# Kernel tuning notes

Hardware: AMD Instinct MI355X
Metric: run time of the kernel (lower is better)

Reference implementation:

```python
import jax, jax.numpy as jnp
import numpy as np

VOCAB, HID, EMB, KSZ, VSZ = 34, 512, 128, 128, 128
T, N, L = 1024, 128, 200


def setup_inputs() -> dict:
    key = jax.random.key(0)
    ks = jax.random.split(key, 20)
    s = 0.05
    emb = jax.random.normal(ks[0], (VOCAB, EMB), jnp.float32) * s
    emb = emb.at[0].set(0.0)  # padding_idx=0
    inp = {
        "key_proj": jax.random.normal(ks[1], (T, N, KSZ), jnp.float32),
        "values": jax.random.normal(ks[2], (T, N, VSZ), jnp.float32),
        "reduced_length": jax.random.randint(ks[3], (N,), 1, T + 1),
        "text": jax.random.randint(ks[4], (N, L), 1, VOCAB),
        "embedding": emb,
        "Wq": jax.random.normal(ks[5], (KSZ, EMB), jnp.float32) * s,
        "bq": jnp.zeros((KSZ,), jnp.float32),
        "W_ih1": jax.random.normal(ks[6], (4 * HID, EMB + VSZ), jnp.float32) * s,
        "W_hh1": jax.random.normal(ks[7], (4 * HID, HID), jnp.float32) * s,
        "b_ih1": jnp.zeros((4 * HID,), jnp.float32),
        "b_hh1": jnp.zeros((4 * HID,), jnp.float32),
        "W_ih2": jax.random.normal(ks[8], (4 * KSZ, HID), jnp.float32) * s,
        "W_hh2": jax.random.normal(ks[9], (4 * KSZ, KSZ), jnp.float32) * s,
        "b_ih2": jnp.zeros((4 * KSZ,), jnp.float32),
        "b_hh2": jnp.zeros((4 * KSZ,), jnp.float32),
        "Wfc": jax.random.normal(ks[10], (EMB, KSZ * 2), jnp.float32) * s,
        "bfc": jnp.zeros((EMB,), jnp.float32),
        "b_out": jnp.zeros((VOCAB,), jnp.float32),
    }
    return inp


def _lstm_cell(x, h, c, Wih, Whh, bih, bhh):
    g = x @ Wih.T + bih + h @ Whh.T + bhh
    i, f, gg, o = jnp.split(g, 4, axis=1)
    c = jax.nn.sigmoid(f) * c + jax.nn.sigmoid(i) * jnp.tanh(gg)
    h = jax.nn.sigmoid(o) * jnp.tanh(c)
    return h, c


def reference(key_proj, values, reduced_length, text, embedding, Wq, bq,
              W_ih1, W_hh1, b_ih1, b_hh1, W_ih2, W_hh2, b_ih2, b_hh2,
              Wfc, bfc, b_out):
    n, l = text.shape
    keyT = jnp.transpose(key_proj, (1, 0, 2))   # (N,T,K)
    valT = jnp.transpose(values, (1, 0, 2))     # (N,T,V)
    t_len = keyT.shape[1]
    mask = jnp.arange(t_len)[None, :] >= reduced_length[:, None]  # (N,T) True=pad

    def attend(q):  # q: (N,K)
        energy = jnp.einsum('ntk,nk->nt', keyT, q)
        energy = jnp.where(mask, -1e9, energy)
        att = jax.nn.softmax(energy, axis=1)
        ctx = jnp.einsum('nt,ntv->nv', att, valT)
        return ctx

    # deterministic teacher forcing: step 0 uses embedding[0] (padding row),
    # step i uses embedding of text[:, i-1]
    char_seq = jnp.concatenate(
        [jnp.broadcast_to(embedding[0], (n, 1, embedding.shape[1])),
         embedding[text[:, :-1]]], axis=1)          # (N,L,E)
    char_seq = jnp.transpose(char_seq, (1, 0, 2))   # (L,N,E)

    h1 = jnp.zeros((n, W_hh1.shape[1]), jnp.float32)
    c1 = jnp.zeros_like(h1)
    h2 = jnp.zeros((n, W_hh2.shape[1]), jnp.float32)
    c2 = jnp.zeros_like(h2)

    def step(carry, ce):
        h1, c1, h2, c2 = carry
        q1 = ce @ Wq.T + bq
        ctx1 = attend(q1)
        inp = jnp.concatenate([ce, ctx1], axis=1)
        h1, c1 = _lstm_cell(inp, h1, c1, W_ih1, W_hh1, b_ih1, b_hh1)
        h2, c2 = _lstm_cell(h1, h2, c2, W_ih2, W_hh2, b_ih2, b_hh2)
        q2 = h2 @ Wq.T + bq
        ctx2 = attend(q2)
        out = jnp.concatenate([h2, ctx2], axis=1) @ Wfc.T + bfc
        out = jnp.clip(out, -1.0, 1.0)  # Hardtanh
        pred = out @ embedding.T + b_out  # tied output weights
        return (h1, c1, h2, c2), pred

    _, preds = jax.lax.scan(step, (h1, c1, h2, c2), char_seq)  # (L,N,V)
    return jnp.transpose(preds, (1, 0, 2))  # (N,L,V)
```

## Files before the change

### kernel.cpp

```cpp
#include <hip/hip_runtime.h>
#include <hip/hip_bf16.h>
#include <math.h>

#define T_LEN 1024
#define NB    128
#define L_SEQ 200
#define EMB   128
#define KSZ   128
#define VSZ   128
#define HID   512
#define G1    2048
#define G2    512
#define VOCAB 34
#define KK1   768
#define KK2   640
#define TT    64
#define NBLK  160
#define GRP_BLKS 40

typedef __attribute__((ext_vector_type(8))) short bf16x8;
typedef __attribute__((ext_vector_type(4))) float f32x4;

__device__ __forceinline__ float sig_(float x) { return 1.0f / (1.0f + __expf(-x)); }
__device__ __forceinline__ float tanh_fast(float x) {
    return 1.0f - 2.0f / (__expf(2.0f * x) + 1.0f);
}

__device__ __forceinline__ f32x4 MFMA_BF16(bf16x8 a, bf16x8 b, f32x4 c) {
    return __builtin_amdgcn_mfma_f32_16x16x32_bf16(a, b, c, 0, 0, 0);
}
__device__ __forceinline__ bf16x8 LD8(const __hip_bfloat16* p) {
    return *(const bf16x8*)p;
}
__device__ __forceinline__ bf16x8 LD8CC(const unsigned int* p) {
    union { bf16x8 v; unsigned long long q[2]; } u;
    unsigned long long* pp = (unsigned long long*)p;
    u.q[0] = __hip_atomic_load(pp,     __ATOMIC_RELAXED, __HIP_MEMORY_SCOPE_AGENT);
    u.q[1] = __hip_atomic_load(pp + 1, __ATOMIC_RELAXED, __HIP_MEMORY_SCOPE_AGENT);
    return u.v;
}
__device__ __forceinline__ void ST4CC(unsigned int* p, unsigned int v) {
    __hip_atomic_store(p, v, __ATOMIC_RELAXED, __HIP_MEMORY_SCOPE_AGENT);
}

__device__ __forceinline__ void gbar_grp(int* bar, int tgt) {
    asm volatile("s_waitcnt vmcnt(0)" ::: "memory");
    __syncthreads();
    if (threadIdx.x == 0) {
        __hip_atomic_fetch_add(bar, 1, __ATOMIC_RELAXED, __HIP_MEMORY_SCOPE_AGENT);
        const long long t0 = __builtin_amdgcn_s_memrealtime();
        while (__hip_atomic_load(bar, __ATOMIC_RELAXED, __HIP_MEMORY_SCOPE_AGENT) < tgt) {
            __builtin_amdgcn_s_sleep(2);
            if (__builtin_amdgcn_s_memrealtime() - t0 > 2000000LL) break;
        }
    }
    __syncthreads();
}

__global__ __launch_bounds__(256) void prep_kernel(
    const float* __restrict__ Wih1, const float* __restrict__ Whh1,
    const float* __restrict__ bih1, const float* __restrict__ bhh1,
    const float* __restrict__ Wih2, const float* __restrict__ Whh2,
    const float* __restrict__ bih2, const float* __restrict__ bhh2,
    __hip_bfloat16* __restrict__ Wc1, __hip_bfloat16* __restrict__ Wc2,
    float* __restrict__ bb1, float* __restrict__ bb2,
    unsigned int* __restrict__ h1x, unsigned int* __restrict__ h2x,
    int* __restrict__ bar)
{
    const int gid = blockIdx.x * 256 + threadIdx.x;
    if (gid < G1 * KK1) {
        const int o = gid / KK1, k = gid - o * KK1;
        const float v = (k < 256) ? Wih1[o * 256 + k] : Whh1[o * 512 + (k - 256)];
        Wc1[gid] = __float2bfloat16(v);
    }
    if (gid < G2 * KK2) {
        const int o = gid / KK2, k = gid - o * KK2;
        const float v = (k < 512) ? Wih2[o * 512 + k] : Whh2[o * 128 + (k - 512)];
        Wc2[gid] = __float2bfloat16(v);
    }
    if (gid < G1) bb1[gid] = bih1[gid] + bhh1[gid];
    if (gid < G2) bb2[gid] = bih2[gid] + bhh2[gid];
    if (gid < 2 * NB * HID / 2) h1x[gid] = 0u;
    if (gid < 2 * NB * KSZ / 2) h2x[gid] = 0u;
    if (gid < 256) bar[gid] = 0;
}

__global__ __launch_bounds__(256) void ce_gather(
    const int* __restrict__ text, const float* __restrict__ emb,
    float* __restrict__ ce_f, __hip_bfloat16* __restrict__ ce_b)
{
    const int idx = blockIdx.x * 256 + threadIdx.x;
    const int k = idx & 127;
    const int rn = idx >> 7;
    const int nn = rn & 127;
    const int s = rn >> 7;
    if (s >= L_SEQ) return;
    const int tok = (s == 0) ? 0 : text[nn * L_SEQ + (s - 1)];
    const float v = emb[(size_t)tok * EMB + k];
    ce_f[idx] = v;
    ce_b[idx] = __float2bfloat16(v);
}

__global__ __launch_bounds__(256) void qproj_kernel(
    const float* __restrict__ src, const float* __restrict__ Wq,
    const float* __restrict__ bq, float* __restrict__ dst)
{
    __shared__ float xs[2][KSZ];
    const int tid = threadIdx.x;
    const int r0 = blockIdx.x * 2;
    xs[tid >> 7][tid & 127] = src[(size_t)(r0 + (tid >> 7)) * KSZ + (tid & 127)];
    __syncthreads();
    const int sub = tid >> 7, o = tid & 127;
    const float* wr = Wq + (size_t)o * KSZ;
    float acc = bq[o];
    #pragma unroll 8
    for (int k = 0; k < KSZ; k += 4) {
        const float4 w4 = *(const float4*)&wr[k];
        const float4 x4 = *(const float4*)&xs[sub][k];
        acc += w4.x * x4.x + w4.y * x4.y + w4.z * x4.z + w4.w * x4.w;
    }
    dst[(size_t)(r0 + sub) * KSZ + o] = acc;
}

__global__ __launch_bounds__(256) void attn_kernel(
    const float* __restrict__ q,
    const float* __restrict__ key,
    const float* __restrict__ values,
    const int* __restrict__ rlen,
    float* __restrict__ ctx_f,
    __hip_bfloat16* __restrict__ ctx_b)
{
    __shared__ __align__(16) float q_s[52][128];
    __shared__ __align__(16) float Kt[TT][129];
    __shared__ __align__(16) float Vt[TT][129];
    __shared__ __align__(16) float es[52][68];
    __shared__ float mm[52], ss[52], al[52];
    const int tid = threadIdx.x;
    const int n = blockIdx.x >> 2;
    const int l0 = (blockIdx.x & 3) * 50;
    const int len = rlen[n];

    for (int idx = tid; idx < 52 * 128; idx += 256) {
        const int l = idx >> 7, k = idx & 127;
        q_s[l][k] = (l < 50) ? q[((size_t)(l0 + l) * NB + n) * KSZ + k] : 0.0f;
    }
    for (int l = tid; l < 52; l += 256) { mm[l] = -3.0e38f; ss[l] = 0.0f; }
    float acc[25];
    #pragma unroll
    for (int j = 0; j < 25; ++j) acc[j] = 0.0f;
    __syncthreads();

    const int lg = tid >> 6, lane = tid & 63;
    const int vv = tid & 127, hh = tid >> 7;
    const int nt = (len + TT - 1) / TT;

    for (int tt = 0; tt < nt; ++tt) {
        const int tb = tt * TT;
        const int valid = min(TT, len - tb);
        #pragma unroll
        for (int it = 0; it < 8; ++it) {
            const int idx4 = tid + it * 256;
            const int r = idx4 >> 5, c4 = (idx4 & 31) * 4;
            float4 kq = make_float4(0.f, 0.f, 0.f, 0.f);
            float4 vq = make_float4(0.f, 0.f, 0.f, 0.f);
            if (r < valid) {
                const size_t base = ((size_t)(tb + r) * NB + n) * 128 + c4;
                kq = *(const float4*)&key[base];
                vq = *(const float4*)&values[base];
            }
            Kt[r][c4 + 0] = kq.x; Kt[r][c4 + 1] = kq.y;
            Kt[r][c4 + 2] = kq.z; Kt[r][c4 + 3] = kq.w;
            Vt[r][c4 + 0] = vq.x; Vt[r][c4 + 1] = vq.y;
            Vt[r][c4 + 2] = vq.z; Vt[r][c4 + 3] = vq.w;
        }
        __syncthreads();
        {
            float e[13];
            #pragma unroll
            for (int j = 0; j < 13; ++j) e[j] = 0.0f;
            for (int k4 = 0; k4 < 128; k4 += 4) {
                const float c0 = Kt[lane][k4 + 0], c1 = Kt[lane][k4 + 1];
                const float c2 = Kt[lane][k4 + 2], c3 = Kt[lane][k4 + 3];
                #pragma unroll
                for (int j = 0; j < 13; ++j) {
                    const float4 q4 = *(const float4*)&q_s[lg * 13 + j][k4];
                    e[j] += c0 * q4.x + c1 * q4.y + c2 * q4.z + c3 * q4.w;
                }
            }
            #pragma unroll
            for (int j = 0; j < 13; ++j) {
                const int l = lg * 13 + j;
                float ev = (lane < valid) ? e[j] : -3.0e38f;
                #pragma unroll
                for (int off = 32; off; off >>= 1) ev = fmaxf(ev, __shfl_xor(ev, off, 64));
                const float mold = mm[l];
                const float mnew = fmaxf(mold, ev);
                const float p = (lane < valid) ? __expf(e[j] - mnew) : 0.0f;
                es[l][lane] = p;
                float ps = p;
                #pragma unroll
                for (int off = 32; off; off >>= 1) ps += __shfl_xor(ps, off, 64);
                if (lane == 0) {
                    const float a = __expf(mold - mnew);
                    al[l] = a;
                    ss[l] = ss[l] * a + ps;
                    mm[l] = mnew;
                }
            }
        }
        __syncthreads();
        #pragma unroll
        for (int j = 0; j < 25; ++j) {
            const int l = hh + 2 * j;
            float a = acc[j] * al[l];
            #pragma unroll 4
            for (int t4 = 0; t4 < TT; t4 += 4) {
                const float4 p4 = *(const float4*)&es[l][t4];
                a += p4.x * Vt[t4 + 0][vv] + p4.y * Vt[t4 + 1][vv]
                   + p4.z * Vt[t4 + 2][vv] + p4.w * Vt[t4 + 3][vv];
            }
            acc[j] = a;
        }
        __syncthreads();
    }
    #pragma unroll
    for (int j = 0; j < 25; ++j) {
        const int l = hh + 2 * j;
        const float r = acc[j] / ss[l];
        const size_t o = ((size_t)(l0 + l) * NB + n) * VSZ + vv;
        ctx_f[o] = r;
        ctx_b[o] = __float2bfloat16(r);
    }
}

__global__ __launch_bounds__(256) void scan_persist(
    const __hip_bfloat16* __restrict__ Wc1, const __hip_bfloat16* __restrict__ Wc2,
    const float* __restrict__ bb1, const float* __restrict__ bb2,
    const __hip_bfloat16* __restrict__ ce_b, const __hip_bfloat16* __restrict__ ctx1_b,
    unsigned int* __restrict__ h1x, unsigned int* __restrict__ h2x,
    float* __restrict__ h2_all, int* __restrict__ bar)
{
    const int tid = threadIdx.x;
    const int w = tid >> 6;
    const int lane = tid & 63;
    const int lrow = lane & 15;
    const int krow = (lane >> 4) * 8;
    __shared__ float gl[4][32][65];
    const int nl = tid >> 3, op = tid & 7;

    if (blockIdx.x < 32) {
        const int grp = blockIdx.x >> 3;
        int* gb = bar + grp * 64;
        const int n0 = grp * 32;
        const int og = blockIdx.x & 7;
        const int wbase = w * 160;
        bf16x8 wf[20];
        #pragma unroll
        for (int t = 0; t < 4; ++t)
            #pragma unroll
            for (int j = 0; j < 5; ++j)
                wf[t * 5 + j] = LD8(Wc2 + (size_t)(t * 128 + og * 16 + lrow) * KK2
                                        + wbase + j * 32 + krow);
        const int oc = og * 16 + 2 * op;
        float bia[4][2];
        #pragma unroll
        for (int g = 0; g < 4; ++g) {
            bia[g][0] = bb2[g * 128 + oc];
            bia[g][1] = bb2[g * 128 + oc + 1];
        }
        float cst0 = 0.0f, cst1 = 0.0f;
        for (int i = 0; i <= L_SEQ; ++i) {
            if (i >= 1) {
                const int s2 = i - 1;
                const int rb = i & 1;
                const unsigned int* h1r = h1x + rb * (NB * HID / 2);
                const unsigned int* h2r = h2x + rb * (NB * KSZ / 2);
                unsigned int* h2w = h2x + (rb ^ 1) * (NB * KSZ / 2);
                f32x4 acc0[4] = {{0,0,0,0},{0,0,0,0},{0,0,0,0},{0,0,0,0}};
                f32x4 acc1[4] = {{0,0,0,0},{0,0,0,0},{0,0,0,0},{0,0,0,0}};
                #pragma unroll
                for (int j = 0; j < 5; ++j) {
                    const int kg = wbase + j * 32 + krow;
                    bf16x8 a0, a1;
                    if (kg < 512) {
                        a0 = LD8CC(h1r + (n0 + lrow) * (HID / 2) + kg / 2);
                        a1 = LD8CC(h1r + (n0 + lrow + 16) * (HID / 2) + kg / 2);
                    } else {
                        a0 = LD8CC(h2r + (n0 + lrow) * (KSZ / 2) + (kg - 512) / 2);
                        a1 = LD8CC(h2r + (n0 + lrow + 16) * (KSZ / 2) + (kg - 512) / 2);
                    }
                    #pragma unroll
                    for (int t = 0; t < 4; ++t) {
                        acc0[t] = MFMA_BF16(a0, wf[t * 5 + j], acc0[t]);
                        acc1[t] = MFMA_BF16(a1, wf[t * 5 + j], acc1[t]);
                    }
                }
                const int rbase = (lane >> 4) * 4;
                #pragma unroll
                for (int t = 0; t < 4; ++t)
                    #pragma unroll
                    for (int r = 0; r < 4; ++r) {
                        gl[w][rbase + r][t * 16 + lrow] = acc0[t][r];
                        gl[w][16 + rbase + r][t * 16 + lrow] = acc1[t][r];
                    }
                __syncthreads();
                float hv0, hv1;
                {
                    float sg[4][2];
                    #pragma unroll
                    for (int g = 0; g < 4; ++g)
                        #pragma unroll
                        for (int cc = 0; cc < 2; ++cc)
                            sg[g][cc] = gl[0][nl][g * 16 + 2 * op + cc]
                                      + gl[1][nl][g * 16 + 2 * op + cc]
                                      + gl[2][nl][g * 16 + 2 * op + cc]
                                      + gl[3][nl][g * 16 + 2 * op + cc] + bia[g][cc];
                    const float cn0 = sig_(sg[1][0]) * cst0 + sig_(sg[0][0]) * tanh_fast(sg[2][0]);
                    const float cn1 = sig_(sg[1][1]) * cst1 + sig_(sg[0][1]) * tanh_fast(sg[2][1]);
                    hv0 = sig_(sg[3][0]) * tanh_fast(cn0);
                    hv1 = sig_(sg[3][1]) * tanh_fast(cn1);
                    cst0 = cn0; cst1 = cn1;
                }
                const int nn = n0 + nl;
                union { unsigned int u; __hip_bfloat16 b[2]; } pk;
                pk.b[0] = __float2bfloat16(hv0);
                pk.b[1] = __float2bfloat16(hv1);
                ST4CC(h2w + nn * (KSZ / 2) + oc / 2, pk.u);
                *(float2*)&h2_all[((size_t)s2 * NB + nn) * KSZ + oc] = make_float2(hv0, hv1);
            }
            if (i < L_SEQ) gbar_grp(gb, GRP_BLKS * (i + 1));
        }
    } else {
        const int bid2 = blockIdx.x - 32;
        const int grp = bid2 >> 5;
        int* gb = bar + grp * 64;
        const int n0 = grp * 32;
        const int og = bid2 & 31;
        const int wbase = w * 192;
        bf16x8 wf[24];
        #pragma unroll
        for (int t = 0; t < 4; ++t)
            #pragma unroll
            for (int j = 0; j < 6; ++j)
                wf[t * 6 + j] = LD8(Wc1 + (size_t)(t * 512 + og * 16 + lrow) * KK1
                                        + wbase + j * 32 + krow);
        const int oc = og * 16 + 2 * op;
        float bia[4][2];
        #pragma unroll
        for (int g = 0; g < 4; ++g) {
            bia[g][0] = bb1[g * 512 + oc];
            bia[g][1] = bb1[g * 512 + oc + 1];
        }
        float cst0 = 0.0f, cst1 = 0.0f;
        for (int i = 0; i < L_SEQ; ++i) {
            const int rb = i & 1;
            const unsigned int* h1r = h1x + rb * (NB * HID / 2);
            unsigned int* h1w = h1x + (rb ^ 1) * (NB * HID / 2);
            f32x4 acc0[4] = {{0,0,0,0},{0,0,0,0},{0,0,0,0},{0,0,0,0}};
            f32x4 acc1[4] = {{0,0,0,0},{0,0,0,0},{0,0,0,0},{0,0,0,0}};
            #pragma unroll
            for (int j = 0; j < 6; ++j) {
                const int kg = wbase + j * 32 + krow;
                bf16x8 a0, a1;
                if (kg < 128) {
                    a0 = LD8(ce_b + ((size_t)i * NB + n0 + lrow) * EMB + kg);
                    a1 = LD8(ce_b + ((size_t)i * NB + n0 + lrow + 16) * EMB + kg);
                } else if (kg < 256) {
                    a0 = LD8(ctx1_b + ((size_t)i * NB + n0 + lrow) * VSZ + kg - 128);
                    a1 = LD8(ctx1_b + ((size_t)i * NB + n0 + lrow + 16) * VSZ + kg - 128);
                } else {
                    a0 = LD8CC(h1r + (n0 + lrow) * (HID / 2) + (kg - 256) / 2);
                    a1 = LD8CC(h1r + (n0 + lrow + 16) * (HID / 2) + (kg - 256) / 2);
                }
                #pragma unroll
                for (int t = 0; t < 4; ++t) {
                    acc0[t] = MFMA_BF16(a0, wf[t * 6 + j], acc0[t]);
                    acc1[t] = MFMA_BF16(a1, wf[t * 6 + j], acc1[t]);
                }
            }
            const int rbase = (lane >> 4) * 4;
            #pragma unroll
            for (int t = 0; t < 4; ++t)
                #pragma unroll
                for (int r = 0; r < 4; ++r) {
                    gl[w][rbase + r][t * 16 + lrow] = acc0[t][r];
                    gl[w][16 + rbase + r][t * 16 + lrow] = acc1[t][r];
                }
            __syncthreads();
            float hv0, hv1;
            {
                float sg[4][2];
                #pragma unroll
                for (int g = 0; g < 4; ++g)
                    #pragma unroll
                    for (int cc = 0; cc < 2; ++cc)
                        sg[g][cc] = gl[0][nl][g * 16 + 2 * op + cc]
                                  + gl[1][nl][g * 16 + 2 * op + cc]
                                  + gl[2][nl][g * 16 + 2 * op + cc]
                                  + gl[3][nl][g * 16 + 2 * op + cc] + bia[g][cc];
                const float cn0 = sig_(sg[1][0]) * cst0 + sig_(sg[0][0]) * tanh_fast(sg[2][0]);
                const float cn1 = sig_(sg[1][1]) * cst1 + sig_(sg[0][1]) * tanh_fast(sg[2][1]);
                hv0 = sig_(sg[3][0]) * tanh_fast(cn0);
                hv1 = sig_(sg[3][1]) * tanh_fast(cn1);
                cst0 = cn0; cst1 = cn1;
            }
            union { unsigned int u; __hip_bfloat16 b[2]; } pk;
            pk.b[0] = __float2bfloat16(hv0);
            pk.b[1] = __float2bfloat16(hv1);
            ST4CC(h1w + (n0 + nl) * (HID / 2) + oc / 2, pk.u);
            gbar_grp(gb, GRP_BLKS * (i + 1));
        }
    }
}

__global__ __launch_bounds__(256) void outpred_kernel(
    const float* __restrict__ h2_all, const float* __restrict__ ctx2,
    const float* __restrict__ Wfc, const float* __restrict__ bfc,
    const float* __restrict__ emb, const float* __restrict__ b_out,
    float* __restrict__ out)
{
    __shared__ float xs[2][256];
    __shared__ float os[2][EMB];
    const int tid = threadIdx.x;
    const int r0 = blockIdx.x * 2;
    const int sub = tid >> 7, lane = tid & 127;
    const int r = r0 + sub;
    xs[sub][lane] = h2_all[(size_t)r * KSZ + lane];
    xs[sub][128 + lane] = ctx2[(size_t)r * VSZ + lane];
    __syncthreads();
    const float* wr = Wfc + (size_t)lane * 256;
    float acc = bfc[lane];
    #pragma unroll 8
    for (int k = 0; k < 256; k += 4) {
        const float4 w4 = *(const float4*)&wr[k];
        const float4 x4 = *(const float4*)&xs[sub][k];
        acc += w4.x * x4.x + w4.y * x4.y + w4.z * x4.z + w4.w * x4.w;
    }
    acc = fminf(1.0f, fmaxf(-1.0f, acc));
    os[sub][lane] = acc;
    __syncthreads();
    if (lane < VOCAB) {
        const float* er = emb + (size_t)lane * EMB;
        float a = b_out[lane];
        #pragma unroll 8
        for (int e = 0; e < EMB; e += 4) {
            const float4 e4 = *(const float4*)&er[e];
            const float4 x4 = *(const float4*)&os[sub][e];
            a += e4.x * x4.x + e4.y * x4.y + e4.z * x4.z + e4.w * x4.w;
        }
        const int s = r >> 7, nn = r & 127;
        out[((size_t)nn * L_SEQ + s) * VOCAB + lane] = a;
    }
}

extern "C" void kernel_launch(void* const* d_in, const int* in_sizes, int n_in,
                              void* d_out, int out_size, void* d_ws, size_t ws_size,
                              hipStream_t stream)
{
    (void)in_sizes; (void)n_in; (void)out_size; (void)ws_size;
    const float* key_proj = (const float*)d_in[0];
    const float* values   = (const float*)d_in[1];
    const int*   rlen     = (const int*)d_in[2];
    const int*   text     = (const int*)d_in[3];
    const float* emb      = (const float*)d_in[4];
    const float* Wq    = (const float*)d_in[5];
    const float* bq    = (const float*)d_in[6];
    const float* Wih1  = (const float*)d_in[7];
    const float* Whh1  = (const float*)d_in[8];
    const float* bih1  = (const float*)d_in[9];
    const float* bhh1  = (const float*)d_in[10];
    const float* Wih2  = (const float*)d_in[11];
    const float* Whh2  = (const float*)d_in[12];
    const float* bih2  = (const float*)d_in[13];
    const float* bhh2  = (const float*)d_in[14];
    const float* Wfc   = (const float*)d_in[15];
    const float* bfc   = (const float*)d_in[16];
    const float* b_out = (const float*)d_in[17];
    float* out = (float*)d_out;

    char* p = (char*)d_ws;
    auto take = [&p](size_t bytes) -> char* {
        char* r = p;
        p += (bytes + 255) & ~((size_t)255);
        return r;
    };
    float* ce_f  = (float*)take((size_t)L_SEQ * NB * EMB * 4);
    __hip_bfloat16* ce_b  = (__hip_bfloat16*)take((size_t)L_SEQ * NB * EMB * 2);
    __hip_bfloat16* ctx_b = (__hip_bfloat16*)take((size_t)L_SEQ * NB * VSZ * 2);
    float* ctx_f  = (float*)take((size_t)L_SEQ * NB * VSZ * 4);
    float* qbuf   = (float*)take((size_t)L_SEQ * NB * KSZ * 4);
    float* h2_all = (float*)take((size_t)L_SEQ * NB * KSZ * 4);
    __hip_bfloat16* Wc1 = (__hip_bfloat16*)take((size_t)G1 * KK1 * 2);
    __hip_bfloat16* Wc2 = (__hip_bfloat16*)take((size_t)G2 * KK2 * 2);
    float* bb1 = (float*)take(G1 * 4);
    float* bb2 = (float*)take(G2 * 4);
    unsigned int* h1x = (unsigned int*)take((size_t)2 * NB * HID / 2 * 4);
    unsigned int* h2x = (unsigned int*)take((size_t)2 * NB * KSZ / 2 * 4);
    int* bar = (int*)take(1024);

    prep_kernel<<<6144, 256, 0, stream>>>(Wih1, Whh1, bih1, bhh1, Wih2, Whh2,
                                          bih2, bhh2, Wc1, Wc2, bb1, bb2,
                                          h1x, h2x, bar);
    ce_gather<<<12800, 256, 0, stream>>>(text, emb, ce_f, ce_b);
    qproj_kernel<<<12800, 256, 0, stream>>>(ce_f, Wq, bq, qbuf);
    attn_kernel<<<512, 256, 0, stream>>>(qbuf, key_proj, values, rlen, ctx_f, ctx_b);
    scan_persist<<<NBLK, 256, 0, stream>>>(Wc1, Wc2, bb1, bb2, ce_b, ctx_b,
                                           h1x, h2x, h2_all, bar);
    qproj_kernel<<<12800, 256, 0, stream>>>(h2_all, Wq, bq, qbuf);
    attn_kernel<<<512, 256, 0, stream>>>(qbuf, key_proj, values, rlen, ctx_f, ctx_b);
    outpred_kernel<<<12800, 256, 0, stream>>>(h2_all, ctx_f, Wfc, bfc, emb, b_out, out);
}
```

Measured before the change: 3.770 ms.

## Replace group barrier with split producer/consumer counters in persistent LSTM scan

The single 40-block group barrier in the persistent scan is replaced by per-subgroup arrival counters. Layer-1 blocks signal one of four counters, layer-2 blocks signal read-done and write-done counters, and each side spins only on the counters it depends on. Layer-1 blocks now prefetch the non-recurrent ce/ctx operands before waiting, and the K-split across warps is reorganised so each warp loads its recurrent slice up front. The attention PV loop is also reordered so each V value is loaded once and reused across 25 rows. This loosens the lockstep between layers to hide synchronisation latency, at the cost of more complex counter protocols and more atomic polling.

```diff
diff --git a/kernel.cpp b/kernel.cpp
--- a/kernel.cpp
+++ b/kernel.cpp
@@ -16,7 +16,6 @@
 #define KK2   640
 #define TT    64
 #define NBLK  160
-#define GRP_BLKS 40
 
 typedef __attribute__((ext_vector_type(8))) short bf16x8;
 typedef __attribute__((ext_vector_type(4))) float f32x4;
@@ -25,7 +24,6 @@
 __device__ __forceinline__ float tanh_fast(float x) {
     return 1.0f - 2.0f / (__expf(2.0f * x) + 1.0f);
 }
-
 __device__ __forceinline__ f32x4 MFMA_BF16(bf16x8 a, bf16x8 b, f32x4 c) {
     return __builtin_amdgcn_mfma_f32_16x16x32_bf16(a, b, c, 0, 0, 0);
 }
@@ -42,19 +40,21 @@
 __device__ __forceinline__ void ST4CC(unsigned int* p, unsigned int v) {
     __hip_atomic_store(p, v, __ATOMIC_RELAXED, __HIP_MEMORY_SCOPE_AGENT);
 }
-
-__device__ __forceinline__ void gbar_grp(int* bar, int tgt) {
-    asm volatile("s_waitcnt vmcnt(0)" ::: "memory");
-    __syncthreads();
-    if (threadIdx.x == 0) {
-        __hip_atomic_fetch_add(bar, 1, __ATOMIC_RELAXED, __HIP_MEMORY_SCOPE_AGENT);
-        const long long t0 = __builtin_amdgcn_s_memrealtime();
-        while (__hip_atomic_load(bar, __ATOMIC_RELAXED, __HIP_MEMORY_SCOPE_AGENT) < tgt) {
-            __builtin_amdgcn_s_sleep(2);
-            if (__builtin_amdgcn_s_memrealtime() - t0 > 2000000LL) break;
-        }
-    }
-    __syncthreads();
+__device__ __forceinline__ void CADD(int* p) {
+    __hip_atomic_fetch_add(p, 1, __ATOMIC_RELAXED, __HIP_MEMORY_SCOPE_AGENT);
+}
+__device__ __forceinline__ void spinw(int* gb, int t1, int tR, int slotR) {
+    const long long t0 = __builtin_amdgcn_s_memrealtime();
+    for (;;) {
+        const int a = __hip_atomic_load(gb +   0, __ATOMIC_RELAXED, __HIP_MEMORY_SCOPE_AGENT);
+        const int b = __hip_atomic_load(gb +  64, __ATOMIC_RELAXED, __HIP_MEMORY_SCOPE_AGENT);
+        const int c = __hip_atomic_load(gb + 128, __ATOMIC_RELAXED, __HIP_MEMORY_SCOPE_AGENT);
+        const int d = __hip_atomic_load(gb + 192, __ATOMIC_RELAXED, __HIP_MEMORY_SCOPE_AGENT);
+        const int r = __hip_atomic_load(gb + slotR * 64, __ATOMIC_RELAXED, __HIP_MEMORY_SCOPE_AGENT);
+        if (a >= t1 && b >= t1 && c >= t1 && d >= t1 && r >= tR) return;
+        __builtin_amdgcn_s_sleep(1);
+        if (__builtin_amdgcn_s_memrealtime() - t0 > 2000000LL) return;
+    }
 }
 
 __global__ __launch_bounds__(256) void prep_kernel(
@@ -82,7 +82,7 @@
     if (gid < G2) bb2[gid] = bih2[gid] + bhh2[gid];
     if (gid < 2 * NB * HID / 2) h1x[gid] = 0u;
     if (gid < 2 * NB * KSZ / 2) h2x[gid] = 0u;
-    if (gid < 256) bar[gid] = 0;
+    if (gid < 2048) bar[gid] = 0;
 }
 
 __global__ __launch_bounds__(256) void ce_gather(
@@ -210,16 +210,15 @@
         }
         __syncthreads();
         #pragma unroll
-        for (int j = 0; j < 25; ++j) {
-            const int l = hh + 2 * j;
-            float a = acc[j] * al[l];
-            #pragma unroll 4
-            for (int t4 = 0; t4 < TT; t4 += 4) {
-                const float4 p4 = *(const float4*)&es[l][t4];
-                a += p4.x * Vt[t4 + 0][vv] + p4.y * Vt[t4 + 1][vv]
-                   + p4.z * Vt[t4 + 2][vv] + p4.w * Vt[t4 + 3][vv];
-            }
-            acc[j] = a;
+        for (int j = 0; j < 25; ++j) acc[j] *= al[hh + 2 * j];
+        for (int t4 = 0; t4 < TT; t4 += 4) {
+            const float v0 = Vt[t4 + 0][vv], v1 = Vt[t4 + 1][vv];
+            const float v2 = Vt[t4 + 2][vv], v3 = Vt[t4 + 3][vv];
+            #pragma unroll
+            for (int j = 0; j < 25; ++j) {
+                const float4 p4 = *(const float4*)&es[hh + 2 * j][t4];
+                acc[j] += p4.x * v0 + p4.y * v1 + p4.z * v2 + p4.w * v3;
+            }
         }
         __syncthreads();
     }
@@ -245,22 +244,23 @@
     const int lane = tid & 63;
     const int lrow = lane & 15;
     const int krow = (lane >> 4) * 8;
-    __shared__ float gl[4][32][65];
+    const int rbase = (lane >> 4) * 4;
+    __shared__ float gl[4][32][68];
     const int nl = tid >> 3, op = tid & 7;
 
     if (blockIdx.x < 32) {
         const int grp = blockIdx.x >> 3;
-        int* gb = bar + grp * 64;
+        int* gb = bar + grp * 6 * 64;
         const int n0 = grp * 32;
         const int og = blockIdx.x & 7;
-        const int wbase = w * 160;
         bf16x8 wf[20];
         #pragma unroll
         for (int t = 0; t < 4; ++t)
             #pragma unroll
-            for (int j = 0; j < 5; ++j)
-                wf[t * 5 + j] = LD8(Wc2 + (size_t)(t * 128 + og * 16 + lrow) * KK2
-                                        + wbase + j * 32 + krow);
+            for (int j = 0; j < 5; ++j) {
+                const int kk = (j < 4) ? (w * 128 + j * 32 + krow) : (512 + w * 32 + krow);
+                wf[t * 5 + j] = LD8(Wc2 + (size_t)(t * 128 + og * 16 + lrow) * KK2 + kk);
+            }
         const int oc = og * 16 + 2 * op;
         float bia[4][2];
         #pragma unroll
@@ -269,116 +269,41 @@
             bia[g][1] = bb2[g * 128 + oc + 1];
         }
         float cst0 = 0.0f, cst1 = 0.0f;
-        for (int i = 0; i <= L_SEQ; ++i) {
-            if (i >= 1) {
-                const int s2 = i - 1;
-                const int rb = i & 1;
-                const unsigned int* h1r = h1x + rb * (NB * HID / 2);
-                const unsigned int* h2r = h2x + rb * (NB * KSZ / 2);
-                unsigned int* h2w = h2x + (rb ^ 1) * (NB * KSZ / 2);
-                f32x4 acc0[4] = {{0,0,0,0},{0,0,0,0},{0,0,0,0},{0,0,0,0}};
-                f32x4 acc1[4] = {{0,0,0,0},{0,0,0,0},{0,0,0,0},{0,0,0,0}};
-                #pragma unroll
-                for (int j = 0; j < 5; ++j) {
-                    const int kg = wbase + j * 32 + krow;
-                    bf16x8 a0, a1;
-                    if (kg < 512) {
-                        a0 = LD8CC(h1r + (n0 + lrow) * (HID / 2) + kg / 2);
-                        a1 = LD8CC(h1r + (n0 + lrow + 16) * (HID / 2) + kg / 2);
-                    } else {
-                        a0 = LD8CC(h2r + (n0 + lrow) * (KSZ / 2) + (kg - 512) / 2);
-                        a1 = LD8CC(h2r + (n0 + lrow + 16) * (KSZ / 2) + (kg - 512) / 2);
-                    }
-                    #pragma unroll
-                    for (int t = 0; t < 4; ++t) {
-                        acc0[t] = MFMA_BF16(a0, wf[t * 5 + j], acc0[t]);
-                        acc1[t] = MFMA_BF16(a1, wf[t * 5 + j], acc1[t]);
-                    }
-                }
-                const int rbase = (lane >> 4) * 4;
-                #pragma unroll
-                for (int t = 0; t < 4; ++t)
-                    #pragma unroll
-                    for (int r = 0; r < 4; ++r) {
-                        gl[w][rbase + r][t * 16 + lrow] = acc0[t][r];
-                        gl[w][16 + rbase + r][t * 16 + lrow] = acc1[t][r];
-                    }
-                __syncthreads();
-                float hv0, hv1;
-                {
-                    float sg[4][2];
-                    #pragma unroll
-                    for (int g = 0; g < 4; ++g)
-                        #pragma unroll
-                        for (int cc = 0; cc < 2; ++cc)
-                            sg[g][cc] = gl[0][nl][g * 16 + 2 * op + cc]
-                                      + gl[1][nl][g * 16 + 2 * op + cc]
-                                      + gl[2][nl][g * 16 + 2 * op + cc]
-                                      + gl[3][nl][g * 16 + 2 * op + cc] + bia[g][cc];
-                    const float cn0 = sig_(sg[1][0]) * cst0 + sig_(sg[0][0]) * tanh_fast(sg[2][0]);
-                    const float cn1 = sig_(sg[1][1]) * cst1 + sig_(sg[0][1]) * tanh_fast(sg[2][1]);
-                    hv0 = sig_(sg[3][0]) * tanh_fast(cn0);
-                    hv1 = sig_(sg[3][1]) * tanh_fast(cn1);
-                    cst0 = cn0; cst1 = cn1;
-                }
-                const int nn = n0 + nl;
-                union { unsigned int u; __hip_bfloat16 b[2]; } pk;
-                pk.b[0] = __float2bfloat16(hv0);
-                pk.b[1] = __float2bfloat16(hv1);
-                ST4CC(h2w + nn * (KSZ / 2) + oc / 2, pk.u);
-                *(float2*)&h2_all[((size_t)s2 * NB + nn) * KSZ + oc] = make_float2(hv0, hv1);
-            }
-            if (i < L_SEQ) gbar_grp(gb, GRP_BLKS * (i + 1));
-        }
-    } else {
-        const int bid2 = blockIdx.x - 32;
-        const int grp = bid2 >> 5;
-        int* gb = bar + grp * 64;
-        const int n0 = grp * 32;
-        const int og = bid2 & 31;
-        const int wbase = w * 192;
-        bf16x8 wf[24];
-        #pragma unroll
-        for (int t = 0; t < 4; ++t)
-            #pragma unroll
-            for (int j = 0; j < 6; ++j)
-                wf[t * 6 + j] = LD8(Wc1 + (size_t)(t * 512 + og * 16 + lrow) * KK1
-                                        + wbase + j * 32 + krow);
-        const int oc = og * 16 + 2 * op;
-        float bia[4][2];
-        #pragma unroll
-        for (int g = 0; g < 4; ++g) {
-            bia[g][0] = bb1[g * 512 + oc];
-            bia[g][1] = bb1[g * 512 + oc + 1];
-        }
-        float cst0 = 0.0f, cst1 = 0.0f;
-        for (int i = 0; i < L_SEQ; ++i) {
-            const int rb = i & 1;
-            const unsigned int* h1r = h1x + rb * (NB * HID / 2);
-            unsigned int* h1w = h1x + (rb ^ 1) * (NB * HID / 2);
+        const unsigned int* h1e = h1x;
+        const unsigned int* h1o = h1x + NB * HID / 2;
+        const unsigned int* h2e = h2x;
+        const unsigned int* h2o = h2x + NB * KSZ / 2;
+        for (int i = 1; i <= L_SEQ; ++i) {
+            if (tid == 0) spinw(gb, 8 * i, 8 * (i - 1), 5);
+            __syncthreads();
+            const int s2 = i - 1;
+            const unsigned int* h1r = (i & 1) ? h1o : h1e;
+            const unsigned int* h2r = (i & 1) ? h2o : h2e;
+            unsigned int* h2w = (unsigned int*)((i & 1) ? h2e : h2o);
+            const unsigned int* r0 = h1r + (n0 + lrow) * (HID / 2) + (w * 128 + krow) / 2;
+            const unsigned int* r1 = h1r + (n0 + lrow + 16) * (HID / 2) + (w * 128 + krow) / 2;
+            const bf16x8 a00 = LD8CC(r0), a01 = LD8CC(r0 + 16), a02 = LD8CC(r0 + 32), a03 = LD8CC(r0 + 48);
+            const bf16x8 a10 = LD8CC(r1), a11 = LD8CC(r1 + 16), a12 = LD8CC(r1 + 32), a13 = LD8CC(r1 + 48);
+            const bf16x8 g0 = LD8CC(h2r + (n0 + lrow) * (KSZ / 2) + (w * 32 + krow) / 2);
+            const bf16x8 g1 = LD8CC(h2r + (n0 + lrow + 16) * (KSZ / 2) + (w * 32 + krow) / 2);
+            asm volatile("s_waitcnt vmcnt(0)" ::: "memory");
+            __syncthreads();
+            if (tid == 0) CADD(gb + 4 * 64);
             f32x4 acc0[4] = {{0,0,0,0},{0,0,0,0},{0,0,0,0},{0,0,0,0}};
             f32x4 acc1[4] = {{0,0,0,0},{0,0,0,0},{0,0,0,0},{0,0,0,0}};
             #pragma unroll
-            for (int j = 0; j < 6; ++j) {
-                const int kg = wbase + j * 32 + krow;
-                bf16x8 a0, a1;
-                if (kg < 128) {
-                    a0 = LD8(ce_b + ((size_t)i * NB + n0 + lrow) * EMB + kg);
-                    a1 = LD8(ce_b + ((size_t)i * NB + n0 + lrow + 16) * EMB + kg);
-                } else if (kg < 256) {
-                    a0 = LD8(ctx1_b + ((size_t)i * NB + n0 + lrow) * VSZ + kg - 128);
-                    a1 = LD8(ctx1_b + ((size_t)i * NB + n0 + lrow + 16) * VSZ + kg - 128);
-                } else {
-                    a0 = LD8CC(h1r + (n0 + lrow) * (HID / 2) + (kg - 256) / 2);
-                    a1 = LD8CC(h1r + (n0 + lrow + 16) * (HID / 2) + (kg - 256) / 2);
-                }
-                #pragma unroll
-                for (int t = 0; t < 4; ++t) {
-                    acc0[t] = MFMA_BF16(a0, wf[t * 6 + j], acc0[t]);
-                    acc1[t] = MFMA_BF16(a1, wf[t * 6 + j], acc1[t]);
-                }
-            }
-            const int rbase = (lane >> 4) * 4;
+            for (int t = 0; t < 4; ++t) {
+                acc0[t] = MFMA_BF16(a00, wf[t * 5 + 0], acc0[t]);
+                acc0[t] = MFMA_BF16(a01, wf[t * 5 + 1], acc0[t]);
+                acc0[t] = MFMA_BF16(a02, wf[t * 5 + 2], acc0[t]);
+                acc0[t] = MFMA_BF16(a03, wf[t * 5 + 3], acc0[t]);
+                acc0[t] = MFMA_BF16(g0,  wf[t * 5 + 4], acc0[t]);
+                acc1[t] = MFMA_BF16(a10, wf[t * 5 + 0], acc1[t]);
+                acc1[t] = MFMA_BF16(a11, wf[t * 5 + 1], acc1[t]);
+                acc1[t] = MFMA_BF16(a12, wf[t * 5 + 2], acc1[t]);
+                acc1[t] = MFMA_BF16(a13, wf[t * 5 + 3], acc1[t]);
+                acc1[t] = MFMA_BF16(g1,  wf[t * 5 + 4], acc1[t]);
+            }
             #pragma unroll
             for (int t = 0; t < 4; ++t)
                 #pragma unroll
@@ -387,28 +312,127 @@
                     gl[w][16 + rbase + r][t * 16 + lrow] = acc1[t][r];
                 }
             __syncthreads();
-            float hv0, hv1;
-            {
-                float sg[4][2];
+            float sg[4][2];
+            #pragma unroll
+            for (int g = 0; g < 4; ++g) {
+                float2 s0 = *(float2*)&gl[0][nl][g * 16 + 2 * op];
+                float2 s1 = *(float2*)&gl[1][nl][g * 16 + 2 * op];
+                float2 s2_ = *(float2*)&gl[2][nl][g * 16 + 2 * op];
+                float2 s3 = *(float2*)&gl[3][nl][g * 16 + 2 * op];
+                sg[g][0] = s0.x + s1.x + s2_.x + s3.x + bia[g][0];
+                sg[g][1] = s0.y + s1.y + s2_.y + s3.y + bia[g][1];
+            }
+            const float cn0 = sig_(sg[1][0]) * cst0 + sig_(sg[0][0]) * tanh_fast(sg[2][0]);
+            const float cn1 = sig_(sg[1][1]) * cst1 + sig_(sg[0][1]) * tanh_fast(sg[2][1]);
+            const float hv0 = sig_(sg[3][0]) * tanh_fast(cn0);
+            const float hv1 = sig_(sg[3][1]) * tanh_fast(cn1);
+            cst0 = cn0; cst1 = cn1;
+            const int nn = n0 + nl;
+            union { unsigned int u; __hip_bfloat16 b[2]; } pk;
+            pk.b[0] = __float2bfloat16(hv0);
+            pk.b[1] = __float2bfloat16(hv1);
+            ST4CC(h2w + nn * (KSZ / 2) + oc / 2, pk.u);
+            *(float2*)&h2_all[((size_t)s2 * NB + nn) * KSZ + oc] = make_float2(hv0, hv1);
+            asm volatile("s_waitcnt vmcnt(0)" ::: "memory");
+            __syncthreads();
+            if (tid == 0) CADD(gb + 5 * 64);
+        }
+    } else {
+        const int bid2 = blockIdx.x - 32;
+        const int grp = bid2 >> 5;
+        int* gb = bar + grp * 6 * 64;
+        const int n0 = grp * 32;
+        const int og = bid2 & 31;
+        int* myctr = gb + (og >> 3) * 64;
+        bf16x8 wf[24];
+        #pragma unroll
+        for (int t = 0; t < 4; ++t)
+            #pragma unroll
+            for (int j = 0; j < 6; ++j) {
+                const int kk = (j < 2) ? (w * 64 + j * 32 + krow)
+                                       : (256 + w * 128 + (j - 2) * 32 + krow);
+                wf[t * 6 + j] = LD8(Wc1 + (size_t)(t * 512 + og * 16 + lrow) * KK1 + kk);
+            }
+        const int oc = og * 16 + 2 * op;
+        float bia[4][2];
+        #pragma unroll
+        for (int g = 0; g < 4; ++g) {
+            bia[g][0] = bb1[g * 512 + oc];
+            bia[g][1] = bb1[g * 512 + oc + 1];
+        }
+        float cst0 = 0.0f, cst1 = 0.0f;
+        const unsigned int* h1e = h1x;
+        const unsigned int* h1o = h1x + NB * HID / 2;
+        for (int i = 0; i < L_SEQ; ++i) {
+            bf16x8 pj0h0, pj1h0, pj0h1, pj1h1;
+            if (w < 2) {
+                const __hip_bfloat16* s0 = ce_b + ((size_t)i * NB + n0 + lrow) * EMB + w * 64 + krow;
+                const __hip_bfloat16* s1 = ce_b + ((size_t)i * NB + n0 + lrow + 16) * EMB + w * 64 + krow;
+                pj0h0 = LD8(s0); pj1h0 = LD8(s0 + 32);
+                pj0h1 = LD8(s1); pj1h1 = LD8(s1 + 32);
+            } else {
+                const __hip_bfloat16* s0 = ctx1_b + ((size_t)i * NB + n0 + lrow) * VSZ + (w - 2) * 64 + krow;
+                const __hip_bfloat16* s1 = ctx1_b + ((size_t)i * NB + n0 + lrow + 16) * VSZ + (w - 2) * 64 + krow;
+                pj0h0 = LD8(s0); pj1h0 = LD8(s0 + 32);
+                pj0h1 = LD8(s1); pj1h1 = LD8(s1 + 32);
+            }
+            if (i) {
+                if (tid == 0) spinw(gb, 8 * i, 8 * (i - 1), 4);
+                __syncthreads();
+            }
+            const unsigned int* h1r = (i & 1) ? h1o : h1e;
+            unsigned int* h1w = (unsigned int*)((i & 1) ? h1e : h1o);
+            const unsigned int* r0 = h1r + (n0 + lrow) * (HID / 2) + (w * 128 + krow) / 2;
+            const unsigned int* r1 = h1r + (n0 + lrow + 16) * (HID / 2) + (w * 128 + krow) / 2;
+            const bf16x8 a20 = LD8CC(r0), a30 = LD8CC(r0 + 16), a40 = LD8CC(r0 + 32), a50 = LD8CC(r0 + 48);
+            const bf16x8 a21 = LD8CC(r1), a31 = LD8CC(r1 + 16), a41 = LD8CC(r1 + 32), a51 = LD8CC(r1 + 48);
+            f32x4 acc0[4] = {{0,0,0,0},{0,0,0,0},{0,0,0,0},{0,0,0,0}};
+            f32x4 acc1[4] = {{0,0,0,0},{0,0,0,0},{0,0,0,0},{0,0,0,0}};
+            #pragma unroll
+            for (int t = 0; t < 4; ++t) {
+                acc0[t] = MFMA_BF16(pj0h0, wf[t * 6 + 0], acc0[t]);
+                acc0[t] = MFMA_BF16(pj1h0, wf[t * 6 + 1], acc0[t]);
+                acc0[t] = MFMA_BF16(a20, wf[t * 6 + 2], acc0[t]);
+                acc0[t] = MFMA_BF16(a30, wf[t * 6 + 3], acc0[t]);
+                acc0[t] = MFMA_BF16(a40, wf[t * 6 + 4], acc0[t]);
+                acc0[t] = MFMA_BF16(a50, wf[t * 6 + 5], acc0[t]);
+                acc1[t] = MFMA_BF16(pj0h1, wf[t * 6 + 0], acc1[t]);
+                acc1[t] = MFMA_BF16(pj1h1, wf[t * 6 + 1], acc1[t]);
+                acc1[t] = MFMA_BF16(a21, wf[t * 6 + 2], acc1[t]);
+                acc1[t] = MFMA_BF16(a31, wf[t * 6 + 3], acc1[t]);
+                acc1[t] = MFMA_BF16(a41, wf[t * 6 + 4], acc1[t]);
+                acc1[t] = MFMA_BF16(a51, wf[t * 6 + 5], acc1[t]);
+            }
+            #pragma unroll
+            for (int t = 0; t < 4; ++t)
                 #pragma unroll
-                for (int g = 0; g < 4; ++g)
-                    #pragma unroll
-                    for (int cc = 0; cc < 2; ++cc)
-                        sg[g][cc] = gl[0][nl][g * 16 + 2 * op + cc]
-                                  + gl[1][nl][g * 16 + 2 * op + cc]
-                                  + gl[2][nl][g * 16 + 2 * op + cc]
-                                  + gl[3][nl][g * 16 + 2 * op + cc] + bia[g][cc];
-                const float cn0 = sig_(sg[1][0]) * cst0 + sig_(sg[0][0]) * tanh_fast(sg[2][0]);
-                const float cn1 = sig_(sg[1][1]) * cst1 + sig_(sg[0][1]) * tanh_fast(sg[2][1]);
-                hv0 = sig_(sg[3][0]) * tanh_fast(cn0);
-                hv1 = sig_(sg[3][1]) * tanh_fast(cn1);
-                cst0 = cn0; cst1 = cn1;
-            }
+                for (int r = 0; r < 4; ++r) {
+                    gl[w][rbase + r][t * 16 + lrow] = acc0[t][r];
+                    gl[w][16 + rbase + r][t * 16 + lrow] = acc1[t][r];
+                }
+            __syncthreads();
+            float sg[4][2];
+            #pragma unroll
+            for (int g = 0; g < 4; ++g) {
+                float2 s0 = *(float2*)&gl[0][nl][g * 16 + 2 * op];
+                float2 s1 = *(float2*)&gl[1][nl][g * 16 + 2 * op];
+                float2 s2_ = *(float2*)&gl[2][nl][g * 16 + 2 * op];
+                float2 s3 = *(float2*)&gl[3][nl][g * 16 + 2 * op];
+                sg[g][0] = s0.x + s1.x + s2_.x + s3.x + bia[g][0];
+                sg[g][1] = s0.y + s1.y + s2_.y + s3.y + bia[g][1];
+            }
+            const float cn0 = sig_(sg[1][0]) * cst0 + sig_(sg[0][0]) * tanh_fast(sg[2][0]);
+            const float cn1 = sig_(sg[1][1]) * cst1 + sig_(sg[0][1]) * tanh_fast(sg[2][1]);
+            const float hv0 = sig_(sg[3][0]) * tanh_fast(cn0);
+            const float hv1 = sig_(sg[3][1]) * tanh_fast(cn1);
+            cst0 = cn0; cst1 = cn1;
             union { unsigned int u; __hip_bfloat16 b[2]; } pk;
             pk.b[0] = __float2bfloat16(hv0);
             pk.b[1] = __float2bfloat16(hv1);
             ST4CC(h1w + (n0 + nl) * (HID / 2) + oc / 2, pk.u);
-            gbar_grp(gb, GRP_BLKS * (i + 1));
+            asm volatile("s_waitcnt vmcnt(0)" ::: "memory");
+            __syncthreads();
+            if (tid == 0) CADD(myctr);
         }
     }
 }
@@ -496,7 +520,7 @@
     float* bb2 = (float*)take(G2 * 4);
     unsigned int* h1x = (unsigned int*)take((size_t)2 * NB * HID / 2 * 4);
     unsigned int* h2x = (unsigned int*)take((size_t)2 * NB * KSZ / 2 * 4);
-    int* bar = (int*)take(1024);
+    int* bar = (int*)take(8192);
 
     prep_kernel<<<6144, 256, 0, stream>>>(Wih1, Whh1, bih1, bhh1, Wih2, Whh2,
                                           bih2, bhh2, Wc1, Wc2, bb1, bb2,
```

Measured after the change: 3.455 ms. -8.4%, faster.
